# Optimization experiments

Measured on AMD Instinct MI355X. Metric: run time of the kernel, lower is better.

The kernel has to match this reference:

```python
import jax, jax.numpy as jnp
from jax import lax
import numpy as np

N_FEATURES = 64
B, H, W = 2, 64, 64
EPS = 1e-12  # F.normalize default eps


def setup_inputs() -> dict:
    key = jax.random.key(0)
    ks = jax.random.split(key, 10)
    L = N_FEATURES
    s = 0.02
    return {
        "x": jax.random.normal(ks[0], (B, L, H, W), dtype=jnp.float32),
        "conv1_w": jax.random.normal(ks[1], (L, L, 3, 3), dtype=jnp.float32) * s,
        "conv1_b": jax.random.normal(ks[2], (L,), dtype=jnp.float32) * s,
        "conv2_w": jax.random.normal(ks[3], (L, L, 3, 3), dtype=jnp.float32) * s,
        "conv2_b": jax.random.normal(ks[4], (L,), dtype=jnp.float32) * s,
        "wq": jax.random.normal(ks[5], (L, L), dtype=jnp.float32) * s,
        "wk": jax.random.normal(ks[6], (L, L), dtype=jnp.float32) * s,
        "wv": jax.random.normal(ks[7], (L, L), dtype=jnp.float32) * s,
        "wo": jax.random.normal(ks[8], (L, L), dtype=jnp.float32) * s,
        "bo": jax.random.normal(ks[9], (L,), dtype=jnp.float32) * s,
    }


def _conv3x3(h, w, b):
    y = lax.conv_general_dilated(
        h, w, window_strides=(1, 1), padding=((1, 1), (1, 1)),
        dimension_numbers=("NCHW", "OIHW", "NCHW"))
    return y + b[None, :, None, None]


def _l2norm(a):
    return a / jnp.maximum(jnp.linalg.norm(a, axis=-1, keepdims=True), EPS)


def reference(x, conv1_w, conv1_b, conv2_w, conv2_b, wq, wk, wv, wo, bo):
    # embedding: conv3x3 -> relu -> conv3x3
    h = _conv3x3(x, conv1_w, conv1_b)
    h = jax.nn.relu(h)
    h = _conv3x3(h, conv2_w, conv2_b)  # [B, L, H, W]
    b, l, hh, ww = h.shape
    t = h.reshape(b, l, hh * ww).transpose(0, 2, 1)  # [B, HW, L]
    q = _l2norm(t @ wq.T)  # [B, HW, L]
    k = _l2norm(t @ wk.T)
    v = t @ wv.T
    # per-token rank-1 outer product scores: [B, HW, L, L]
    scores = q[..., :, None] * k[..., None, :]
    p = jax.nn.softmax(scores, axis=-1)
    out = jnp.einsum("bncd,bnd->bnc", p, v)  # [B, HW, L]
    out = out @ wo.T + bo
    out = out.transpose(0, 2, 1).reshape(b, l, hh, ww)
    return out + h
```

## Files before the change

kernel.cpp:

```cpp
#include <hip/hip_runtime.h>
#include <hip/hip_bf16.h>


#define IMG 262144

using frag_ab = __attribute__((ext_vector_type(8))) short;
using frag_cd = __attribute__((ext_vector_type(4))) float;
typedef unsigned u32x4 __attribute__((ext_vector_type(4)));
typedef float    f32x2 __attribute__((ext_vector_type(2)));
typedef float    f32x4 __attribute__((ext_vector_type(4)));

static __device__ inline unsigned short f2bf(float f) {
    unsigned u = __float_as_uint(f);
    return (unsigned short)((u + 0x7FFFu + ((u >> 16) & 1u)) >> 16);
}
static __device__ inline float bflo(unsigned p) { return __uint_as_float(p << 16); }
static __device__ inline float bfhi(unsigned p) { return __uint_as_float(p & 0xFFFF0000u); }

#if __has_builtin(__builtin_amdgcn_fdot2_f32_bf16)
typedef __bf16 bf16x2 __attribute__((ext_vector_type(2)));
static __device__ inline float dot2bf(unsigned a, unsigned b, float c) {
    union U { unsigned u; bf16x2 v; };
    U ua, ub; ua.u = a; ub.u = b;
    return __builtin_amdgcn_fdot2_f32_bf16(ua.v, ub.v, c, false);
}
#else
static __device__ inline float dot2bf(unsigned a, unsigned b, float c) {
    return fmaf(bflo(a), bflo(b), fmaf(bfhi(a), bfhi(b), c));
}
#endif

#if __has_builtin(__builtin_amdgcn_exp2f)
#define EXP2F(x) __builtin_amdgcn_exp2f(x)
#else
#define EXP2F(x) __expf(0.6931471805599453f * (x))
#endif

__global__ __launch_bounds__(256) void prep_w(
    const float* __restrict__ w1, const float* __restrict__ w2,
    const float* __restrict__ wq, const float* __restrict__ wk,
    const float* __restrict__ wv, const float* __restrict__ wo,
    unsigned short* __restrict__ wt1, unsigned short* __restrict__ wt2,
    unsigned* __restrict__ wp)
{
    int i = blockIdx.x * 256 + threadIdx.x;
    if (i < 73728) {
        int mat = i >= 36864;
        int j = i - mat * 36864;
        int tap = j >> 12;
        int oc  = (j >> 6) & 63;
        int ic  = j & 63;
        const float* w = mat ? w2 : w1;
        int g = oc >> 4, m = oc & 15;
        int s = ic >> 5, q = (ic >> 3) & 3, e = ic & 7;
        int dst = ((((tap * 4 + g) * 2 + s) * 4 + q) * 16 + m) * 8 + e;
        (mat ? wt2 : wt1)[dst] = f2bf(w[(oc * 64 + ic) * 9 + tap]);
    } else {
        int a = i - 73728;
        int mat = a >> 11;
        int r = a & 2047;
        int c = r >> 5, dp = r & 31;
        const float* w = (mat == 0) ? wq : (mat == 1) ? wk : (mat == 2) ? wv : wo;
        unsigned val = (unsigned)f2bf(w[c * 64 + 2 * dp]) |
                       ((unsigned)f2bf(w[c * 64 + 2 * dp + 1]) << 16);
        wp[((mat * 8 + (dp >> 2)) * 64 + c) * 4 + (dp & 3)] = val;
    }
}

__global__ __launch_bounds__(256, 3) void fused_k(
    const float* __restrict__ x,
    const unsigned short* __restrict__ wt1, const unsigned short* __restrict__ wt2,
    const float* __restrict__ b1, const float* __restrict__ b2,
    const unsigned* __restrict__ wp, const float* __restrict__ bo,
    float* __restrict__ out)
{
    __shared__ __align__(16) unsigned short xt[5 * 20 * 72];
    __shared__ __align__(16) unsigned short r1[54 * 72];
    __shared__ __align__(16) float          t_lds[16 * 66];
    __shared__ __align__(16) unsigned       tp[16 * 32];
    __shared__ __align__(16) f32x2          kv[16 * 64];
    __shared__ __align__(16) unsigned short o_l[16 * 64];

    const int tid  = threadIdx.x;
    const int b    = blockIdx.x >> 8;
    const int y    = (blockIdx.x >> 2) & 63;
    const int x0   = (blockIdx.x & 3) * 16;
    const int wv_  = tid >> 6;
    const int lane = tid & 63;
    const int m    = lane & 15;
    const int q    = lane >> 4;
    const int oc0  = wv_ * 16;

    frag_ab A1[9][2];
    #pragma unroll
    for (int t = 0; t < 9; ++t)
        #pragma unroll
        for (int s = 0; s < 2; ++s)
            A1[t][s] = *(const frag_ab*)&wt1[(((t * 4 + wv_) * 2 + s) * 64 + lane) * 8];

    {
        const int xl  = tid & 15;
        const int sub = tid >> 4;
        #pragma unroll
        for (int i = 0; i < 20; ++i) {
            int pair = i * 16 + sub;
            int row = pair >> 6, ic = pair & 63;
            int yy = y - 2 + row;
            int yc = min(max(yy, 0), 63);
            float f = x[((b * 64 + ic) * 64 + yc) * 64 + x0 + xl];
            unsigned short v = f2bf(f);
            if (yy != yc) v = 0;
            xt[(row * 20 + xl + 2) * 72 + ic] = v;
        }
        #pragma unroll
        for (int j = 0; j < 5; ++j) {
            int e = j * 256 + tid;
            int col = e & 3, pair = e >> 2;
            int row = pair >> 6, ic = pair & 63;
            int xsl = (col < 2) ? col : col + 16;
            int gx = x0 - 2 + xsl;
            int gxc = min(max(gx, 0), 63);
            int yy = y - 2 + row;
            int yc = min(max(yy, 0), 63);
            float f = x[((b * 64 + ic) * 64 + yc) * 64 + gxc];
            unsigned short v = f2bf(f);
            if (yy != yc || gx != gxc) v = 0;
            xt[(row * 20 + xsl) * 72 + ic] = v;
        }
    }
    __syncthreads();

    int pb[4], rn_[4], xs_[4];
    bool nv[4];
    #pragma unroll
    for (int nt = 0; nt < 4; ++nt) {
        int n  = nt * 16 + m;
        int nc = min(n, 53);
        int rr = nc / 18, xx = nc - rr * 18;
        rn_[nt] = rr; xs_[nt] = xx; nv[nt] = (n < 54);
        pb[nt] = (rr * 20 + xx) * 72 + q * 8;
    }
    frag_cd acc1[4];
    #pragma unroll
    for (int i = 0; i < 4; ++i) acc1[i] = (frag_cd){0.f, 0.f, 0.f, 0.f};

    #pragma unroll
    for (int ky = 0; ky < 3; ++ky)
        #pragma unroll
        for (int kx = 0; kx < 3; ++kx)
            #pragma unroll
            for (int s = 0; s < 2; ++s) {
                frag_ab a = A1[ky * 3 + kx][s];
                int off = (ky * 20 + kx) * 72 + s * 32;
                #pragma unroll
                for (int nt = 0; nt < 4; ++nt)
                    acc1[nt] = __builtin_amdgcn_mfma_f32_16x16x32_bf16(
                        a, *(const frag_ab*)&xt[pb[nt] + off], acc1[nt], 0, 0, 0);
            }

    frag_ab A2[9][2];
    #pragma unroll
    for (int t = 0; t < 9; ++t)
        #pragma unroll
        for (int s = 0; s < 2; ++s)
            A2[t][s] = *(const frag_ab*)&wt2[(((t * 4 + wv_) * 2 + s) * 64 + lane) * 8];

    {
        frag_cd b1f = *(const frag_cd*)&b1[oc0 + q * 4];
        #pragma unroll
        for (int nt = 0; nt < 4; ++nt) {
            if (!nv[nt]) continue;
            int n = nt * 16 + m;
            int gy = y - 1 + rn_[nt];
            int gx = x0 - 1 + xs_[nt];
            bool oob = (gy < 0) | (gy > 63) | (gx < 0) | (gx > 63);
            #pragma unroll
            for (int r = 0; r < 4; ++r) {
                float v = fmaxf(acc1[nt][r] + b1f[r], 0.f);
                r1[n * 72 + oc0 + q * 4 + r] = oob ? (unsigned short)0 : f2bf(v);
            }
        }
    }
    __syncthreads();

    frag_cd acc2 = (frag_cd){0.f, 0.f, 0.f, 0.f};
    #pragma unroll
    for (int ky = 0; ky < 3; ++ky)
        #pragma unroll
        for (int kx = 0; kx < 3; ++kx)
            #pragma unroll
            for (int s = 0; s < 2; ++s)
                acc2 = __builtin_amdgcn_mfma_f32_16x16x32_bf16(
                    A2[ky * 3 + kx][s],
                    *(const frag_ab*)&r1[(ky * 18 + m + kx) * 72 + s * 32 + q * 8],
                    acc2, 0, 0, 0);

    {
        frag_cd b2f = *(const frag_cd*)&b2[oc0 + q * 4];
        float hv[4];
        #pragma unroll
        for (int r = 0; r < 4; ++r) {
            hv[r] = acc2[r] + b2f[r];
            t_lds[m * 66 + oc0 + q * 4 + r] = hv[r];
        }
        int dpb = (oc0 >> 1) + q * 2;
        tp[m * 32 + dpb + 0] = (unsigned)f2bf(hv[0]) | ((unsigned)f2bf(hv[1]) << 16);
        tp[m * 32 + dpb + 1] = (unsigned)f2bf(hv[2]) | ((unsigned)f2bf(hv[3]) << 16);
    }
    __syncthreads();

    const float bo_c = bo[lane];
    const int t0_ = wv_ * 4;

    float qq[4] = {0,0,0,0}, kk[4] = {0,0,0,0}, vv[4] = {0,0,0,0};
    #pragma unroll
    for (int dp4 = 0; dp4 < 8; ++dp4) {
        u32x4 pq = *(const u32x4*)&wp[(dp4 * 64 + lane) * 4];
        u32x4 pk = *(const u32x4*)&wp[((8 + dp4) * 64 + lane) * 4];
        u32x4 pv = *(const u32x4*)&wp[((16 + dp4) * 64 + lane) * 4];
        #pragma unroll
        for (int i = 0; i < 4; ++i) {
            u32x4 tpv = *(const u32x4*)&tp[(t0_ + i) * 32 + dp4 * 4];
            #pragma unroll
            for (int j = 0; j < 4; ++j) {
                qq[i] = dot2bf(pq[j], tpv[j], qq[i]);
                kk[i] = dot2bf(pk[j], tpv[j], kk[i]);
                vv[i] = dot2bf(pv[j], tpv[j], vv[i]);
            }
        }
    }

    float nq[4], nk[4];
    #pragma unroll
    for (int i = 0; i < 4; ++i) { nq[i] = qq[i] * qq[i]; nk[i] = kk[i] * kk[i]; }
    #pragma unroll
    for (int s = 32; s > 0; s >>= 1)
        #pragma unroll
        for (int i = 0; i < 4; ++i) {
            nq[i] += __shfl_xor(nq[i], s);
            nk[i] += __shfl_xor(nk[i], s);
        }
    #pragma unroll
    for (int i = 0; i < 4; ++i) {
        qq[i] = qq[i] / fmaxf(sqrtf(nq[i]), 1e-12f) * 1.44269504f;
        kk[i] = kk[i] / fmaxf(sqrtf(nk[i]), 1e-12f);
        kv[(t0_ + i) * 64 + lane] = (f32x2){kk[i], vv[i]};
    }

    float den[4] = {0,0,0,0}, num[4] = {0,0,0,0};
    #pragma unroll 4
    for (int d2 = 0; d2 < 32; ++d2) {
        #pragma unroll
        for (int i = 0; i < 4; ++i) {
            f32x4 K = *(const f32x4*)&kv[(t0_ + i) * 64 + d2 * 2];
            float e0 = EXP2F(qq[i] * K[0]); den[i] += e0; num[i] = fmaf(e0, K[1], num[i]);
            float e1 = EXP2F(qq[i] * K[2]); den[i] += e1; num[i] = fmaf(e1, K[3], num[i]);
        }
    }
    #pragma unroll
    for (int i = 0; i < 4; ++i)
        o_l[(t0_ + i) * 64 + lane] = f2bf(num[i] / den[i]);

    float res[4], po[4];
    #pragma unroll
    for (int i = 0; i < 4; ++i) {
        res[i] = t_lds[(t0_ + i) * 66 + lane];
        po[i]  = bo_c;
    }
    #pragma unroll
    for (int dp4 = 0; dp4 < 8; ++dp4) {
        u32x4 pw = *(const u32x4*)&wp[((24 + dp4) * 64 + lane) * 4];
        #pragma unroll
        for (int i = 0; i < 4; ++i) {
            u32x4 ov = *(const u32x4*)&o_l[(t0_ + i) * 64 + dp4 * 8];
            #pragma unroll
            for (int j = 0; j < 4; ++j)
                po[i] = dot2bf(pw[j], ov[j], po[i]);
        }
    }
    #pragma unroll
    for (int i = 0; i < 4; ++i)
        t_lds[(t0_ + i) * 66 + lane] = po[i] + res[i];
    __syncthreads();

    {
        int c = tid >> 2, xg = tid & 3;
        f32x4 o4;
        #pragma unroll
        for (int j = 0; j < 4; ++j) o4[j] = t_lds[(xg * 4 + j) * 66 + c];
        *(f32x4*)&out[((b * 64 + c) * 64 + y) * 64 + x0 + xg * 4] = o4;
    }
}

extern "C" void kernel_launch(void* const* d_in, const int* in_sizes, int n_in,
                              void* d_out, int out_size, void* d_ws, size_t ws_size,
                              hipStream_t stream) {
    const float* x  = (const float*)d_in[0];
    const float* w1 = (const float*)d_in[1];
    const float* b1 = (const float*)d_in[2];
    const float* w2 = (const float*)d_in[3];
    const float* b2 = (const float*)d_in[4];
    const float* wq = (const float*)d_in[5];
    const float* wk = (const float*)d_in[6];
    const float* wv = (const float*)d_in[7];
    const float* wo = (const float*)d_in[8];
    const float* bo = (const float*)d_in[9];
    float* out = (float*)d_out;

    unsigned*       wpp = (unsigned*)d_ws;
    unsigned short* wt1 = (unsigned short*)((char*)d_ws + 32768);
    unsigned short* wt2 = wt1 + 36864;

    prep_w<<<320, 256, 0, stream>>>(w1, w2, wq, wk, wv, wo, wt1, wt2, wpp);
    fused_k<<<512, 256, 0, stream>>>(x, wt1, wt2, b1, b2, wpp, bo, out);
}
```

Before: 94.79 us.

## Move QKV and output projections onto MFMA and vectorize input tile loads

Replaces the per-lane bf16 dot2 projections for q/k/v and the output projection with 16x16x32 bf16 MFMA instructions, repacking the small weight matrices into MFMA fragment layout in the prep kernel. Norms are now reduced across waves through a small LDS buffer. The softmax loop is reorganised per token row instead of per lane, and the input halo is loaded with float4 vector loads. Output is written straight from MFMA fragments rather than through an LDS transpose. Occupancy hint drops from 3 to 2 blocks because the extra weight fragments raise register use, and the direct output stores are less coalesced.

```diff
diff --git a/kernel.cpp b/kernel.cpp
--- a/kernel.cpp
+++ b/kernel.cpp
@@ -14,21 +14,9 @@
     unsigned u = __float_as_uint(f);
     return (unsigned short)((u + 0x7FFFu + ((u >> 16) & 1u)) >> 16);
 }
-static __device__ inline float bflo(unsigned p) { return __uint_as_float(p << 16); }
-static __device__ inline float bfhi(unsigned p) { return __uint_as_float(p & 0xFFFF0000u); }
-
-#if __has_builtin(__builtin_amdgcn_fdot2_f32_bf16)
-typedef __bf16 bf16x2 __attribute__((ext_vector_type(2)));
-static __device__ inline float dot2bf(unsigned a, unsigned b, float c) {
-    union U { unsigned u; bf16x2 v; };
-    U ua, ub; ua.u = a; ub.u = b;
-    return __builtin_amdgcn_fdot2_f32_bf16(ua.v, ub.v, c, false);
-}
-#else
-static __device__ inline float dot2bf(unsigned a, unsigned b, float c) {
-    return fmaf(bflo(a), bflo(b), fmaf(bfhi(a), bfhi(b), c));
-}
-#endif
+static __device__ inline unsigned packbf(float a, float b) {
+    return (unsigned)f2bf(a) | ((unsigned)f2bf(b) << 16);
+}
 
 #if __has_builtin(__builtin_amdgcn_exp2f)
 #define EXP2F(x) __builtin_amdgcn_exp2f(x)
@@ -41,7 +29,7 @@
     const float* __restrict__ wq, const float* __restrict__ wk,
     const float* __restrict__ wv, const float* __restrict__ wo,
     unsigned short* __restrict__ wt1, unsigned short* __restrict__ wt2,
-    unsigned* __restrict__ wp)
+    unsigned short* __restrict__ wa)
 {
     int i = blockIdx.x * 256 + threadIdx.x;
     if (i < 73728) {
@@ -51,35 +39,40 @@
         int oc  = (j >> 6) & 63;
         int ic  = j & 63;
         const float* w = mat ? w2 : w1;
-        int g = oc >> 4, m = oc & 15;
-        int s = ic >> 5, q = (ic >> 3) & 3, e = ic & 7;
-        int dst = ((((tap * 4 + g) * 2 + s) * 4 + q) * 16 + m) * 8 + e;
+        int g = oc >> 4, mm = oc & 15;
+        int s = ic >> 5, qq = (ic >> 3) & 3, e = ic & 7;
+        int dst = ((((tap * 4 + g) * 2 + s) * 4 + qq) * 16 + mm) * 8 + e;
         (mat ? wt2 : wt1)[dst] = f2bf(w[(oc * 64 + ic) * 9 + tap]);
     } else {
         int a = i - 73728;
-        int mat = a >> 11;
-        int r = a & 2047;
-        int c = r >> 5, dp = r & 31;
+        int mat = a >> 12;
+        int j = a & 4095;
+        int e    = j & 7;
+        int lane = (j >> 3) & 63;
+        int gs   = j >> 9;
+        int g = gs >> 1, s = gs & 1;
+        int qq = lane >> 4, mm = lane & 15;
+        int oc = 16 * g + mm;
+        int ic = 32 * s + 8 * qq + e;
         const float* w = (mat == 0) ? wq : (mat == 1) ? wk : (mat == 2) ? wv : wo;
-        unsigned val = (unsigned)f2bf(w[c * 64 + 2 * dp]) |
-                       ((unsigned)f2bf(w[c * 64 + 2 * dp + 1]) << 16);
-        wp[((mat * 8 + (dp >> 2)) * 64 + c) * 4 + (dp & 3)] = val;
-    }
-}
-
-__global__ __launch_bounds__(256, 3) void fused_k(
+        wa[mat * 4096 + j] = f2bf(w[oc * 64 + ic]);
+    }
+}
+
+__global__ __launch_bounds__(256, 2) void fused_k(
     const float* __restrict__ x,
     const unsigned short* __restrict__ wt1, const unsigned short* __restrict__ wt2,
     const float* __restrict__ b1, const float* __restrict__ b2,
-    const unsigned* __restrict__ wp, const float* __restrict__ bo,
+    const unsigned short* __restrict__ wa, const float* __restrict__ bo,
     float* __restrict__ out)
 {
     __shared__ __align__(16) unsigned short xt[5 * 20 * 72];
     __shared__ __align__(16) unsigned short r1[54 * 72];
-    __shared__ __align__(16) float          t_lds[16 * 66];
-    __shared__ __align__(16) unsigned       tp[16 * 32];
-    __shared__ __align__(16) f32x2          kv[16 * 64];
-    __shared__ __align__(16) unsigned short o_l[16 * 64];
+    __shared__ __align__(16) float          t_lds[16 * 68];
+    __shared__ __align__(16) unsigned       tp[16 * 36];
+    __shared__ __align__(16) f32x2          kv[16 * 66];
+    __shared__ __align__(16) unsigned       o_l32[16 * 36];
+    __shared__ __align__(16) f32x2          nrm[4 * 17];
 
     const int tid  = threadIdx.x;
     const int b    = blockIdx.x >> 8;
@@ -88,7 +81,7 @@
     const int wv_  = tid >> 6;
     const int lane = tid & 63;
     const int m    = lane & 15;
-    const int q    = lane >> 4;
+    const int qd   = lane >> 4;
     const int oc0  = wv_ * 16;
 
     frag_ab A1[9][2];
@@ -98,34 +91,25 @@
         for (int s = 0; s < 2; ++s)
             A1[t][s] = *(const frag_ab*)&wt1[(((t * 4 + wv_) * 2 + s) * 64 + lane) * 8];
 
-    {
-        const int xl  = tid & 15;
-        const int sub = tid >> 4;
-        #pragma unroll
-        for (int i = 0; i < 20; ++i) {
-            int pair = i * 16 + sub;
-            int row = pair >> 6, ic = pair & 63;
-            int yy = y - 2 + row;
-            int yc = min(max(yy, 0), 63);
-            float f = x[((b * 64 + ic) * 64 + yc) * 64 + x0 + xl];
-            unsigned short v = f2bf(f);
-            if (yy != yc) v = 0;
-            xt[(row * 20 + xl + 2) * 72 + ic] = v;
-        }
-        #pragma unroll
-        for (int j = 0; j < 5; ++j) {
-            int e = j * 256 + tid;
-            int col = e & 3, pair = e >> 2;
-            int row = pair >> 6, ic = pair & 63;
-            int xsl = (col < 2) ? col : col + 16;
-            int gx = x0 - 2 + xsl;
-            int gxc = min(max(gx, 0), 63);
-            int yy = y - 2 + row;
-            int yc = min(max(yy, 0), 63);
-            float f = x[((b * 64 + ic) * 64 + yc) * 64 + gxc];
-            unsigned short v = f2bf(f);
-            if (yy != yc || gx != gxc) v = 0;
-            xt[(row * 20 + xsl) * 72 + ic] = v;
+    #pragma unroll
+    for (int it = 0; it < 10; ++it) {
+        int e    = it * 256 + tid;
+        int grp  = e & 7;
+        int pair = e >> 3;
+        int row = pair >> 6, ic = pair & 63;
+        int yy = y - 2 + row;
+        int yc = min(max(yy, 0), 63);
+        int gx0 = x0 - 8 + grp * 4;
+        int gxl = min(max(gx0, 0), 60);
+        f32x4 v = *(const f32x4*)&x[((b * 64 + ic) * 64 + yc) * 64 + gxl];
+        #pragma unroll
+        for (int j = 0; j < 4; ++j) {
+            int gx  = gx0 + j;
+            int xsl = gx - x0 + 2;
+            if (xsl < 0 || xsl >= 20) continue;
+            unsigned short val =
+                (yy == yc && gx >= 0 && gx <= 63) ? f2bf(v[j]) : (unsigned short)0;
+            xt[(row * 20 + xsl) * 72 + ic] = val;
         }
     }
     __syncthreads();
@@ -138,7 +122,7 @@
         int nc = min(n, 53);
         int rr = nc / 18, xx = nc - rr * 18;
         rn_[nt] = rr; xs_[nt] = xx; nv[nt] = (n < 54);
-        pb[nt] = (rr * 20 + xx) * 72 + q * 8;
+        pb[nt] = (rr * 20 + xx) * 72 + qd * 8;
     }
     frag_cd acc1[4];
     #pragma unroll
@@ -164,9 +148,18 @@
         #pragma unroll
         for (int s = 0; s < 2; ++s)
             A2[t][s] = *(const frag_ab*)&wt2[(((t * 4 + wv_) * 2 + s) * 64 + lane) * 8];
+    frag_ab Aq[2], Ak[2], Av[2], Ao[2];
+    #pragma unroll
+    for (int s = 0; s < 2; ++s) {
+        int off = ((wv_ * 2 + s) * 64 + lane) * 8;
+        Aq[s] = *(const frag_ab*)&wa[off];
+        Ak[s] = *(const frag_ab*)&wa[4096 + off];
+        Av[s] = *(const frag_ab*)&wa[8192 + off];
+        Ao[s] = *(const frag_ab*)&wa[12288 + off];
+    }
 
     {
-        frag_cd b1f = *(const frag_cd*)&b1[oc0 + q * 4];
+        frag_cd b1f = *(const frag_cd*)&b1[oc0 + qd * 4];
         #pragma unroll
         for (int nt = 0; nt < 4; ++nt) {
             if (!nv[nt]) continue;
@@ -177,7 +170,7 @@
             #pragma unroll
             for (int r = 0; r < 4; ++r) {
                 float v = fmaxf(acc1[nt][r] + b1f[r], 0.f);
-                r1[n * 72 + oc0 + q * 4 + r] = oob ? (unsigned short)0 : f2bf(v);
+                r1[n * 72 + oc0 + qd * 4 + r] = oob ? (unsigned short)0 : f2bf(v);
             }
         }
     }
@@ -192,103 +185,80 @@
             for (int s = 0; s < 2; ++s)
                 acc2 = __builtin_amdgcn_mfma_f32_16x16x32_bf16(
                     A2[ky * 3 + kx][s],
-                    *(const frag_ab*)&r1[(ky * 18 + m + kx) * 72 + s * 32 + q * 8],
+                    *(const frag_ab*)&r1[(ky * 18 + m + kx) * 72 + s * 32 + qd * 8],
                     acc2, 0, 0, 0);
 
     {
-        frag_cd b2f = *(const frag_cd*)&b2[oc0 + q * 4];
-        float hv[4];
+        frag_cd b2f = *(const frag_cd*)&b2[oc0 + qd * 4];
+        f32x4 hv;
+        #pragma unroll
+        for (int r = 0; r < 4; ++r) hv[r] = acc2[r] + b2f[r];
+        *(f32x4*)&t_lds[m * 68 + oc0 + qd * 4] = hv;
+        int dpb = m * 36 + (oc0 >> 1) + qd * 2;
+        tp[dpb + 0] = packbf(hv[0], hv[1]);
+        tp[dpb + 1] = packbf(hv[2], hv[3]);
+    }
+    __syncthreads();
+
+    frag_cd qA = (frag_cd){0,0,0,0}, kA = (frag_cd){0,0,0,0}, vA = (frag_cd){0,0,0,0};
+    #pragma unroll
+    for (int s = 0; s < 2; ++s) {
+        frag_ab hfrag = *(const frag_ab*)&tp[m * 36 + s * 16 + qd * 4];
+        qA = __builtin_amdgcn_mfma_f32_16x16x32_bf16(Aq[s], hfrag, qA, 0, 0, 0);
+        kA = __builtin_amdgcn_mfma_f32_16x16x32_bf16(Ak[s], hfrag, kA, 0, 0, 0);
+        vA = __builtin_amdgcn_mfma_f32_16x16x32_bf16(Av[s], hfrag, vA, 0, 0, 0);
+    }
+
+    float nq = qA[0]*qA[0] + qA[1]*qA[1] + qA[2]*qA[2] + qA[3]*qA[3];
+    float nk = kA[0]*kA[0] + kA[1]*kA[1] + kA[2]*kA[2] + kA[3]*kA[3];
+    nq += __shfl_xor(nq, 16); nq += __shfl_xor(nq, 32);
+    nk += __shfl_xor(nk, 16); nk += __shfl_xor(nk, 32);
+    if (qd == 0) nrm[wv_ * 17 + m] = (f32x2){nq, nk};
+    __syncthreads();
+    f32x2 p0 = nrm[m],      p1 = nrm[17 + m];
+    f32x2 p2 = nrm[34 + m], p3 = nrm[51 + m];
+    float snq = p0.x + p1.x + p2.x + p3.x;
+    float snk = p0.y + p1.y + p2.y + p3.y;
+    float rq = 1.4426950408889634f / fmaxf(sqrtf(snq), 1e-12f);
+    float rk = 1.0f / fmaxf(sqrtf(snk), 1e-12f);
+
+    float qn[4];
+    #pragma unroll
+    for (int r = 0; r < 4; ++r) {
+        qn[r] = qA[r] * rq;
+        kv[m * 66 + oc0 + qd * 4 + r] = (f32x2){kA[r] * rk, vA[r]};
+    }
+    __syncthreads();
+
+    float den[4] = {0, 0, 0, 0}, num[4] = {0, 0, 0, 0};
+    #pragma unroll 8
+    for (int d2 = 0; d2 < 32; ++d2) {
+        f32x4 K = *(const f32x4*)&kv[m * 66 + d2 * 2];
         #pragma unroll
         for (int r = 0; r < 4; ++r) {
-            hv[r] = acc2[r] + b2f[r];
-            t_lds[m * 66 + oc0 + q * 4 + r] = hv[r];
+            float e0 = EXP2F(qn[r] * K[0]); den[r] += e0; num[r] = fmaf(e0, K[1], num[r]);
+            float e1 = EXP2F(qn[r] * K[2]); den[r] += e1; num[r] = fmaf(e1, K[3], num[r]);
         }
-        int dpb = (oc0 >> 1) + q * 2;
-        tp[m * 32 + dpb + 0] = (unsigned)f2bf(hv[0]) | ((unsigned)f2bf(hv[1]) << 16);
-        tp[m * 32 + dpb + 1] = (unsigned)f2bf(hv[2]) | ((unsigned)f2bf(hv[3]) << 16);
-    }
-    __syncthreads();
-
-    const float bo_c = bo[lane];
-    const int t0_ = wv_ * 4;
-
-    float qq[4] = {0,0,0,0}, kk[4] = {0,0,0,0}, vv[4] = {0,0,0,0};
-    #pragma unroll
-    for (int dp4 = 0; dp4 < 8; ++dp4) {
-        u32x4 pq = *(const u32x4*)&wp[(dp4 * 64 + lane) * 4];
-        u32x4 pk = *(const u32x4*)&wp[((8 + dp4) * 64 + lane) * 4];
-        u32x4 pv = *(const u32x4*)&wp[((16 + dp4) * 64 + lane) * 4];
-        #pragma unroll
-        for (int i = 0; i < 4; ++i) {
-            u32x4 tpv = *(const u32x4*)&tp[(t0_ + i) * 32 + dp4 * 4];
-            #pragma unroll
-            for (int j = 0; j < 4; ++j) {
-                qq[i] = dot2bf(pq[j], tpv[j], qq[i]);
-                kk[i] = dot2bf(pk[j], tpv[j], kk[i]);
-                vv[i] = dot2bf(pv[j], tpv[j], vv[i]);
-            }
-        }
-    }
-
-    float nq[4], nk[4];
-    #pragma unroll
-    for (int i = 0; i < 4; ++i) { nq[i] = qq[i] * qq[i]; nk[i] = kk[i] * kk[i]; }
-    #pragma unroll
-    for (int s = 32; s > 0; s >>= 1)
-        #pragma unroll
-        for (int i = 0; i < 4; ++i) {
-            nq[i] += __shfl_xor(nq[i], s);
-            nk[i] += __shfl_xor(nk[i], s);
-        }
-    #pragma unroll
-    for (int i = 0; i < 4; ++i) {
-        qq[i] = qq[i] / fmaxf(sqrtf(nq[i]), 1e-12f) * 1.44269504f;
-        kk[i] = kk[i] / fmaxf(sqrtf(nk[i]), 1e-12f);
-        kv[(t0_ + i) * 64 + lane] = (f32x2){kk[i], vv[i]};
-    }
-
-    float den[4] = {0,0,0,0}, num[4] = {0,0,0,0};
-    #pragma unroll 4
-    for (int d2 = 0; d2 < 32; ++d2) {
-        #pragma unroll
-        for (int i = 0; i < 4; ++i) {
-            f32x4 K = *(const f32x4*)&kv[(t0_ + i) * 64 + d2 * 2];
-            float e0 = EXP2F(qq[i] * K[0]); den[i] += e0; num[i] = fmaf(e0, K[1], num[i]);
-            float e1 = EXP2F(qq[i] * K[2]); den[i] += e1; num[i] = fmaf(e1, K[3], num[i]);
-        }
-    }
-    #pragma unroll
-    for (int i = 0; i < 4; ++i)
-        o_l[(t0_ + i) * 64 + lane] = f2bf(num[i] / den[i]);
-
-    float res[4], po[4];
-    #pragma unroll
-    for (int i = 0; i < 4; ++i) {
-        res[i] = t_lds[(t0_ + i) * 66 + lane];
-        po[i]  = bo_c;
-    }
-    #pragma unroll
-    for (int dp4 = 0; dp4 < 8; ++dp4) {
-        u32x4 pw = *(const u32x4*)&wp[((24 + dp4) * 64 + lane) * 4];
-        #pragma unroll
-        for (int i = 0; i < 4; ++i) {
-            u32x4 ov = *(const u32x4*)&o_l[(t0_ + i) * 64 + dp4 * 8];
-            #pragma unroll
-            for (int j = 0; j < 4; ++j)
-                po[i] = dot2bf(pw[j], ov[j], po[i]);
-        }
-    }
-    #pragma unroll
-    for (int i = 0; i < 4; ++i)
-        t_lds[(t0_ + i) * 66 + lane] = po[i] + res[i];
-    __syncthreads();
-
+    }
     {
-        int c = tid >> 2, xg = tid & 3;
-        f32x4 o4;
-        #pragma unroll
-        for (int j = 0; j < 4; ++j) o4[j] = t_lds[(xg * 4 + j) * 66 + c];
-        *(f32x4*)&out[((b * 64 + c) * 64 + y) * 64 + x0 + xg * 4] = o4;
+        int ob = m * 36 + wv_ * 8 + qd * 2;
+        o_l32[ob + 0] = packbf(num[0] / den[0], num[1] / den[1]);
+        o_l32[ob + 1] = packbf(num[2] / den[2], num[3] / den[3]);
+    }
+    __syncthreads();
+
+    frag_cd oA = (frag_cd){0, 0, 0, 0};
+    #pragma unroll
+    for (int s = 0; s < 2; ++s)
+        oA = __builtin_amdgcn_mfma_f32_16x16x32_bf16(
+            Ao[s], *(const frag_ab*)&o_l32[m * 36 + s * 16 + qd * 4], oA, 0, 0, 0);
+
+    f32x4 bo4 = *(const f32x4*)&bo[oc0 + qd * 4];
+    f32x4 res = *(const f32x4*)&t_lds[m * 68 + oc0 + qd * 4];
+    #pragma unroll
+    for (int r = 0; r < 4; ++r) {
+        float v = oA[r] + bo4[r] + res[r];
+        out[((b * 64 + oc0 + qd * 4 + r) * 64 + y) * 64 + x0 + m] = v;
     }
 }
 
@@ -307,10 +277,10 @@
     const float* bo = (const float*)d_in[9];
     float* out = (float*)d_out;
 
-    unsigned*       wpp = (unsigned*)d_ws;
+    unsigned short* wa  = (unsigned short*)d_ws;
     unsigned short* wt1 = (unsigned short*)((char*)d_ws + 32768);
     unsigned short* wt2 = wt1 + 36864;
 
-    prep_w<<<320, 256, 0, stream>>>(w1, w2, wq, wk, wv, wo, wt1, wt2, wpp);
-    fused_k<<<512, 256, 0, stream>>>(x, wt1, wt2, b1, b2, wpp, bo, out);
-}
+    prep_w<<<352, 256, 0, stream>>>(w1, w2, wq, wk, wv, wo, wt1, wt2, wa);
+    fused_k<<<512, 256, 0, stream>>>(x, wt1, wt2, b1, b2, wa, bo, out);
+}
```

Measured after the change: 88.19 us. -7.0%, faster.
